# Kernel tuning notes

Hardware: AMD Instinct MI355X
Metric: run time of the kernel (lower is better)

The kernel has to match this reference:

```python
import jax, jax.numpy as jnp
import numpy as np

THRESH = 1.0   # snntorch Leaky default threshold
SLOPE = 25.0   # surrogate.fast_sigmoid(slope=25)
DIM_HEAD = 64
SCALE = DIM_HEAD ** -0.5

# snn.Leaky single step from zero membrane: mem = beta*0 + input = input,
# spike = heaviside(mem - threshold); backward uses fast_sigmoid surrogate.
@jax.custom_vjp
def spike_fn(mem):
    return (mem > THRESH).astype(mem.dtype)

def _spike_fwd(mem):
    return (mem > THRESH).astype(mem.dtype), mem

def _spike_bwd(mem, g):
    return (g / (SLOPE * jnp.abs(mem - THRESH) + 1.0) ** 2,)

spike_fn.defvjp(_spike_fwd, _spike_bwd)

def layer_norm2(x, gamma, beta, eps=1e-5):
    # torch F.layer_norm over x.shape[1:] (last two dims jointly);
    # gamma.repeat(rows,1) == broadcast of gamma over the row axis.
    m = x.mean(axis=(-2, -1), keepdims=True)
    v = x.var(axis=(-2, -1), keepdims=True)
    return (x - m) / jnp.sqrt(v + eps) * gamma + beta

def interp_linear(x, out_len):
    # F.interpolate(mode='linear', align_corners=False) over last axis
    L = x.shape[-1]
    j = jnp.arange(out_len, dtype=x.dtype)
    src = jnp.maximum((j + 0.5) * (L / out_len) - 0.5, 0.0)
    i0 = jnp.clip(jnp.floor(src).astype(jnp.int32), 0, L - 1)
    i1 = jnp.clip(i0 + 1, 0, L - 1)
    w = src - i0.astype(x.dtype)
    return x[..., i0] * (1.0 - w) + x[..., i1] * w

def setup_inputs() -> dict:
    key = jax.random.key(0)
    ks = jax.random.split(key, 8)
    H, N, DIM, HEADS, DH = 4, 512, 8192, 2, 64
    inner = HEADS * DH  # 128; H*inner = 512 (matches fc/conv dims)
    return {
        "pic": jax.random.normal(ks[0], (H, N, DIM), jnp.float32),
        "context": jax.random.normal(ks[1], (H, N, DIM), jnp.float32),
        "gamma": jnp.ones((DIM,), jnp.float32),
        "ln_beta": jnp.zeros((DIM,), jnp.float32),
        "W_pic": jax.random.normal(ks[2], (inner, DIM), jnp.float32) * 0.01,
        "b_pic": jnp.zeros((inner,), jnp.float32),
        "W_ctx": jax.random.normal(ks[3], (2 * DH, DIM), jnp.float32) * 0.01,
        "b_ctx": jnp.zeros((2 * DH,), jnp.float32),
        "conv1_w": jax.random.normal(ks[4], (32, N, 1), jnp.float32) * 0.04,
        "conv1_b": jnp.zeros((32,), jnp.float32),
        "conv2_w": jax.random.normal(ks[5], (1, 32, 1), jnp.float32) * 0.17,
        "conv2_b": jnp.zeros((1,), jnp.float32),
        "fc_w": jax.random.normal(ks[6], (N, N), jnp.float32) * 0.04,
        "fc_b": jnp.zeros((N,), jnp.float32),
    }

def reference(pic, context, gamma, ln_beta, W_pic, b_pic, W_ctx, b_ctx,
              conv1_w, conv1_b, conv2_w, conv2_b, fc_w, fc_b):
    pic = layer_norm2(pic, gamma, ln_beta)          # (H,N,DIM)
    context = layer_norm2(context, gamma, ln_beta)
    # num_steps = batch_size = 1: one SNN step, stack adds leading 'b'=1 axis
    ip_spk = spike_fn(pic)[None]                    # (1,H,N,DIM)
    ic_spk = spike_fn(context)[None]
    ip = (jnp.einsum('bhnd,od->bhno', ip_spk, W_pic) + b_pic) * SCALE  # (1,H,N,128)
    ctx = jnp.einsum('bhnd,od->bhno', ic_spk, W_ctx) + b_ctx           # (1,H,N,128)
    ic, V = jnp.split(ctx, 2, axis=-1)              # (1,H,N,64) each
    # einsum 'b h i d, b h i j -> b h i d': reduce j then broadcast-multiply
    sim = ip * ic.sum(-1, keepdims=True)            # (1,H,N,128)
    attn = jax.nn.softmax(sim, axis=-1)             # (sim - amax then softmax)
    # einsum 'b h i j, b h i d -> b h i j'
    out = attn * V.sum(-1, keepdims=True)           # (1,H,N,128)
    b, h, n, d = out.shape
    out = jnp.transpose(out, (0, 2, 1, 3)).reshape(b, n, h * d)  # (1,512,512)
    ip_sum = ip.sum(axis=3)                         # (1,H,512)
    # resnet: two kernel-size-1 Conv1d == channel-mixing matmuls
    o1 = jnp.einsum('bcl,oc->bol', out, conv1_w[:, :, 0]) + conv1_b[None, :, None]
    o1 = jnp.einsum('bcl,oc->bol', o1, conv2_w[:, :, 0]) + conv2_b[None, :, None]  # (1,1,512)
    o1 = o1 @ fc_w.T + fc_b                         # (1,1,512)
    o1 = o1 + ip_sum                                # broadcast -> (1,H,512)
    o1 = jnp.transpose(o1, (0, 2, 1))               # (1,512,H)
    o1 = interp_linear(o1, 64)                      # (1,512,64)
    ic_sum = ic.sum(axis=1)                         # (1,512,64)
    return jax.nn.relu(jax.nn.relu(o1) + ic_sum)
```

## Files before the change

kernel.cpp:

```cpp
#include <hip/hip_runtime.h>

typedef unsigned short ushort;
typedef unsigned int uint;
typedef __attribute__((ext_vector_type(8))) short short8v;
typedef __attribute__((ext_vector_type(4))) float floatx4;

#define DIMK   8192
#define NPER   512
#define NROWS  2048
#define NCOLS  128
#define KSPLIT 8
#define KCHUNK 1024
#define BK     64
#define BM     64
#define NIT    16
#define SLICE_ELEMS 4194304.0

static const size_t STATS_OFF = 0;
static const size_t O2_OFF    = 128;
static const size_t WB_OFF    = 4096;
static const size_t WB_BYTES  = (size_t)2 * 128 * DIMK * 2;
static const size_t P_OFF     = WB_OFF + WB_BYTES;
static const size_t P_BYTES   = (size_t)2 * KSPLIT * NROWS * NCOLS * 4;
static const size_t OUT2_OFF  = P_OFF + P_BYTES;
static const size_t IPSUM_OFF = OUT2_OFF + (size_t)512 * 512 * 4;
static const size_t CTXB_OFF  = IPSUM_OFF + (size_t)4 * 512 * 4;
static const size_t WS_NEED   = CTXB_OFF + (size_t)2048 * 64 * 4;

__device__ __forceinline__ ushort f2bf(float x) {
  uint u = __float_as_uint(x);
  return (ushort)((u + 0x7FFFu + ((u >> 16) & 1u)) >> 16);
}

__global__ __launch_bounds__(256) void k_wconv(const float* __restrict__ Wp,
                                               const float* __restrict__ Wc,
                                               ushort* __restrict__ Wb) {
  const size_t i = ((size_t)blockIdx.x * 256 + threadIdx.x) * 8;
  const size_t HALF = (size_t)128 * DIMK;
  const float* src = (i < HALF) ? (Wp + i) : (Wc + (i - HALF));
  float4 a = *(const float4*)src;
  float4 b = *(const float4*)(src + 4);
  short8v v;
  v[0] = (short)f2bf(a.x); v[1] = (short)f2bf(a.y);
  v[2] = (short)f2bf(a.z); v[3] = (short)f2bf(a.w);
  v[4] = (short)f2bf(b.x); v[5] = (short)f2bf(b.y);
  v[6] = (short)f2bf(b.z); v[7] = (short)f2bf(b.w);
  *(short8v*)&Wb[i] = v;
}

__global__ __launch_bounds__(256) void k_stats(const float* __restrict__ pic,
                                               const float* __restrict__ ctx,
                                               double* __restrict__ stats) {
  const int bid = blockIdx.x;
  const int tid = threadIdx.x;
  const int s = bid >> 8;
  const int c = bid & 255;
  const int t = s >> 2, h = s & 3;
  const float4* p4 = reinterpret_cast<const float4*>(
      (t ? ctx : pic) + (size_t)h * NPER * DIMK + (size_t)c * 16384) + tid;

  float4 va[4], vb[4];
  float sA[4] = {0.f, 0.f, 0.f, 0.f};
  float qA[4] = {0.f, 0.f, 0.f, 0.f};

  auto ACC = [&](const float4* v) {
#pragma unroll
    for (int j = 0; j < 4; ++j) {
      const float4 w = v[j];
      sA[j] += (w.x + w.y) + (w.z + w.w);
      qA[j] += (w.x * w.x + w.y * w.y) + (w.z * w.z + w.w * w.w);
    }
  };

#pragma unroll
  for (int j = 0; j < 4; ++j) va[j] = p4[256 * j];
#pragma unroll
  for (int j = 0; j < 4; ++j) vb[j] = p4[256 * (4 + j)];
  __builtin_amdgcn_sched_barrier(0);
  ACC(va);
#pragma unroll
  for (int j = 0; j < 4; ++j) va[j] = p4[256 * (8 + j)];
  __builtin_amdgcn_sched_barrier(0);
  ACC(vb);
#pragma unroll
  for (int j = 0; j < 4; ++j) vb[j] = p4[256 * (12 + j)];
  __builtin_amdgcn_sched_barrier(0);
  ACC(va);
  ACC(vb);

  float sum = (sA[0] + sA[1]) + (sA[2] + sA[3]);
  float sq  = (qA[0] + qA[1]) + (qA[2] + qA[3]);
#pragma unroll
  for (int d = 1; d < 64; d <<= 1) {
    sum += __shfl_xor(sum, d);
    sq  += __shfl_xor(sq, d);
  }
  __shared__ float ps[4], pq[4];
  const int w = tid >> 6;
  if ((tid & 63) == 0) { ps[w] = sum; pq[w] = sq; }
  __syncthreads();
  if (tid == 0) {
    double S = (double)ps[0] + (double)ps[1] + (double)ps[2] + (double)ps[3];
    double Q = (double)pq[0] + (double)pq[1] + (double)pq[2] + (double)pq[3];
    atomicAdd(&stats[2 * s], S);
    atomicAdd(&stats[2 * s + 1], Q);
  }
}

__global__ __launch_bounds__(256, 2) void k_gemm(const float* __restrict__ pic,
                                                 const float* __restrict__ ctxin,
                                                 const float* __restrict__ gamma,
                                                 const float* __restrict__ lnbeta,
                                                 const ushort* __restrict__ Wb,
                                                 const double* __restrict__ stats,
                                                 float* __restrict__ P) {
  const int tid  = threadIdx.x;
  const int lane = tid & 63;
  const int wv   = tid >> 6;
  const int wm   = wv >> 1, wn = wv & 1;
  const int bx = blockIdx.x, ky = blockIdx.y, t = blockIdx.z;
  const float*  A  = t ? ctxin : pic;
  const ushort* Wt = Wb + (size_t)t * 128 * DIMK;
  const int row0 = bx * BM;

  const int sidx = t * 4 + (bx >> 3);
  double su = stats[2 * sidx], qu = stats[2 * sidx + 1];
  double dmean = su * (1.0 / SLICE_ELEMS);
  const float mean = (float)dmean;
  const float var  = (float)(qu * (1.0 / SLICE_ELEMS) - dmean * dmean);
  const float rstd = rsqrtf(var + 1e-5f);

  __shared__ __align__(16) ushort Asl[2][BM * BK];
  __shared__ __align__(16) ushort Wsl[2][128 * BK];

  const int k8 = (tid & 7) * 8;
  const int r0 = tid >> 3;

  const int kg8 = (lane >> 4) << 3;
  int abase[2], axor[2], bbase[4], bxor[4];
#pragma unroll
  for (int m = 0; m < 2; ++m) {
    const int ra = wm * 32 + m * 16 + (lane & 15);
    abase[m] = ra * BK; axor[m] = (ra & 7) << 3;
  }
#pragma unroll
  for (int n = 0; n < 4; ++n) {
    const int rb = wn * 64 + n * 16 + (lane & 15);
    bbase[n] = rb * BK; bxor[n] = (rb & 7) << 3;
  }

  floatx4 acc[2][4];
  floatx4 zz = {0.f, 0.f, 0.f, 0.f};
#pragma unroll
  for (int m = 0; m < 2; ++m)
#pragma unroll
    for (int n = 0; n < 4; ++n) acc[m][n] = zz;

  float4 xa[2][2]; uint4 xw[4];
  float4 g0, g1, bb0, bb1;

  auto LOAD = [&](int it) {
    const int kb = ky * KCHUNK + it * BK;
    const float* gp = gamma  + kb + k8;
    const float* bp = lnbeta + kb + k8;
    g0 = *(const float4*)gp;  g1 = *(const float4*)(gp + 4);
    bb0 = *(const float4*)bp; bb1 = *(const float4*)(bp + 4);
#pragma unroll
    for (int c = 0; c < 2; ++c) {
      const float* ap = A + (size_t)(row0 + r0 + c * 32) * DIMK + kb + k8;
      xa[c][0] = *(const float4*)ap;
      xa[c][1] = *(const float4*)(ap + 4);
    }
#pragma unroll
    for (int c = 0; c < 4; ++c)
      xw[c] = *(const uint4*)(Wt + (size_t)(r0 + c * 32) * DIMK + kb + k8);
  };

  auto WRITE = [&](int buf) {
#pragma unroll
    for (int c = 0; c < 2; ++c) {
      const int r = r0 + c * 32;
      float xs[8] = {xa[c][0].x, xa[c][0].y, xa[c][0].z, xa[c][0].w,
                     xa[c][1].x, xa[c][1].y, xa[c][1].z, xa[c][1].w};
      float gs[8] = {g0.x, g0.y, g0.z, g0.w, g1.x, g1.y, g1.z, g1.w};
      float bs[8] = {bb0.x, bb0.y, bb0.z, bb0.w, bb1.x, bb1.y, bb1.z, bb1.w};
      short8v sv;
#pragma unroll
      for (int j = 0; j < 8; ++j)
        sv[j] = (short)(((xs[j] - mean) * rstd * gs[j] + bs[j] > 1.0f) ? 0x3F80 : 0);
      *(short8v*)&Asl[buf][r * BK + (k8 ^ ((r & 7) << 3))] = sv;
    }
#pragma unroll
    for (int c = 0; c < 4; ++c) {
      const int r = r0 + c * 32;
      *(uint4*)&Wsl[buf][r * BK + (k8 ^ ((r & 7) << 3))] = xw[c];
    }
  };

  auto COMPUTE = [&](int buf) {
#pragma unroll
    for (int ks = 0; ks < 2; ++ks) {
      short8v af[2], bfr[4];
#pragma unroll
      for (int m = 0; m < 2; ++m)
        af[m] = *(const short8v*)&Asl[buf][abase[m] + ((ks * 32 + kg8) ^ axor[m])];
#pragma unroll
      for (int n = 0; n < 4; ++n)
        bfr[n] = *(const short8v*)&Wsl[buf][bbase[n] + ((ks * 32 + kg8) ^ bxor[n])];
#pragma unroll
      for (int m = 0; m < 2; ++m)
#pragma unroll
        for (int n = 0; n < 4; ++n)
          acc[m][n] = __builtin_amdgcn_mfma_f32_16x16x32_bf16(af[m], bfr[n], acc[m][n], 0, 0, 0);
    }
  };

  LOAD(0);
  WRITE(0);
  __syncthreads();
#pragma unroll 2
  for (int it = 0; it < NIT - 1; ++it) {
    LOAD(it + 1);
    COMPUTE(it & 1);
    __syncthreads();
    WRITE((it + 1) & 1);
    __syncthreads();
  }
  COMPUTE((NIT - 1) & 1);

  float* Pt = P + ((size_t)(t * KSPLIT + ky) * NROWS + row0) * NCOLS;
#pragma unroll
  for (int m = 0; m < 2; ++m) {
    const int gr = wm * 32 + m * 16 + ((lane >> 4) << 2);
#pragma unroll
    for (int n = 0; n < 4; ++n) {
      const int gc = wn * 64 + n * 16 + (lane & 15);
#pragma unroll
      for (int j = 0; j < 4; ++j)
        Pt[(size_t)(gr + j) * NCOLS + gc] = acc[m][n][j];
    }
  }
}

__global__ __launch_bounds__(256) void k_row(const float* __restrict__ P,
                                             const float* __restrict__ b_pic,
                                             const float* __restrict__ b_ctx,
                                             float* __restrict__ out2,
                                             float* __restrict__ ipsum,
                                             float* __restrict__ ctxbuf) {
  const int tid = threadIdx.x;
  const int q = tid >> 5;
  const int u = tid & 31;
  const int r = blockIdx.x * 8 + q;
  const int o4 = u * 4;

  float4 ip = ((const float4*)b_pic)[u];
  float4 cv = ((const float4*)b_ctx)[u];
#pragma unroll
  for (int ks = 0; ks < KSPLIT; ++ks) {
    const float4 a = *(const float4*)&P[((size_t)ks * NROWS + r) * NCOLS + o4];
    const float4 b = *(const float4*)&P[((size_t)(KSPLIT + ks) * NROWS + r) * NCOLS + o4];
    ip.x += a.x; ip.y += a.y; ip.z += a.z; ip.w += a.w;
    cv.x += b.x; cv.y += b.y; cv.z += b.z; cv.w += b.w;
  }
  ip.x *= 0.125f; ip.y *= 0.125f; ip.z *= 0.125f; ip.w *= 0.125f;

  float clo = (u < 16) ? (cv.x + cv.y) + (cv.z + cv.w) : 0.f;
  float chi = (u >= 16) ? (cv.x + cv.y) + (cv.z + cv.w) : 0.f;
  float ipp = (ip.x + ip.y) + (ip.z + ip.w);
#pragma unroll
  for (int d = 1; d < 32; d <<= 1) {
    clo += __shfl_xor(clo, d);
    chi += __shfl_xor(chi, d);
    ipp += __shfl_xor(ipp, d);
  }
  const float ic_s = clo, v_s = chi;
  if (u == 0) ipsum[r] = ipp;

  float4 sim;
  sim.x = ip.x * ic_s; sim.y = ip.y * ic_s; sim.z = ip.z * ic_s; sim.w = ip.w * ic_s;
  float m = fmaxf(fmaxf(sim.x, sim.y), fmaxf(sim.z, sim.w));
#pragma unroll
  for (int d = 1; d < 32; d <<= 1) m = fmaxf(m, __shfl_xor(m, d));
  float4 e;
  e.x = __expf(sim.x - m); e.y = __expf(sim.y - m);
  e.z = __expf(sim.z - m); e.w = __expf(sim.w - m);
  float es = (e.x + e.y) + (e.z + e.w);
#pragma unroll
  for (int d = 1; d < 32; d <<= 1) es += __shfl_xor(es, d);
  const float sc = v_s / es;
  float4 outv;
  outv.x = e.x * sc; outv.y = e.y * sc; outv.z = e.z * sc; outv.w = e.w * sc;

  const int hh = r >> 9, n = r & 511;
  *(float4*)&out2[(size_t)n * 512 + hh * 128 + o4] = outv;
  if (u < 16) *(float4*)&ctxbuf[(size_t)r * 64 + o4] = cv;
}

__global__ __launch_bounds__(512) void k_mid(const float* __restrict__ out2,
                                             const float* __restrict__ c1w,
                                             const float* __restrict__ c1b,
                                             const float* __restrict__ c2w,
                                             const float* __restrict__ c2b,
                                             float* __restrict__ o2buf) {
  const int b = blockIdx.x;
  const int tid = threadIdx.x;
  __shared__ float wsh[64];
  __shared__ float c2s[32];
  if (tid < 32) c2s[tid] = c2w[tid];
  __syncthreads();
  if (tid < 64) {
    const int n = b * 64 + tid;
    float a = 0.f;
#pragma unroll
    for (int o = 0; o < 32; ++o) a += c2s[o] * c1w[o * 512 + n];
    wsh[tid] = a;
  }
  __syncthreads();
  float acc = 0.f;
#pragma unroll 8
  for (int ucnt = 0; ucnt < 64; ++ucnt)
    acc += out2[(size_t)(b * 64 + ucnt) * 512 + tid] * wsh[ucnt];
  if (b == 0) {
    float beff = c2b[0];
#pragma unroll
    for (int o = 0; o < 32; ++o) beff += c2s[o] * c1b[o];
    acc += beff;
  }
  atomicAdd(&o2buf[tid], acc);
}

__global__ __launch_bounds__(64) void k_final(const float* __restrict__ o2buf,
                                              const float* __restrict__ fcw,
                                              const float* __restrict__ fcb,
                                              const float* __restrict__ ipsum,
                                              const float* __restrict__ ctxbuf,
                                              float* __restrict__ out) {
  const int i = blockIdx.x;
  const int j = threadIdx.x;
  float a = 0.f;
#pragma unroll
  for (int uu = 0; uu < 8; ++uu) {
    const int k = j * 8 + uu;
    a += o2buf[k] * fcw[(size_t)i * 512 + k];
  }
#pragma unroll
  for (int d = 1; d < 64; d <<= 1) a += __shfl_xor(a, d);
  const float o3 = a + fcb[i];

  float src = (j + 0.5f) * (4.0f / 64.0f) - 0.5f;
  src = fmaxf(src, 0.0f);
  int i0 = (int)floorf(src);
  if (i0 > 3) i0 = 3;
  const int i1 = (i0 + 1 < 3) ? i0 + 1 : 3;
  const float w = src - (float)i0;

  const float v0 = o3 + ipsum[i0 * 512 + i];
  const float v1 = o3 + ipsum[i1 * 512 + i];
  float v = v0 * (1.0f - w) + v1 * w;
  v = fmaxf(v, 0.0f);

  float ics = 0.f;
#pragma unroll
  for (int hh2 = 0; hh2 < 4; ++hh2) ics += ctxbuf[((size_t)hh2 * 512 + i) * 64 + j];
  out[(size_t)i * 64 + j] = fmaxf(v + ics, 0.0f);
}

extern "C" void kernel_launch(void* const* d_in, const int* in_sizes, int n_in,
                              void* d_out, int out_size, void* d_ws, size_t ws_size,
                              hipStream_t stream) {
  const float* pic    = (const float*)d_in[0];
  const float* ctx    = (const float*)d_in[1];
  const float* gamma  = (const float*)d_in[2];
  const float* lnbeta = (const float*)d_in[3];
  const float* Wp     = (const float*)d_in[4];
  const float* bp     = (const float*)d_in[5];
  const float* Wc     = (const float*)d_in[6];
  const float* bc     = (const float*)d_in[7];
  const float* c1w    = (const float*)d_in[8];
  const float* c1b    = (const float*)d_in[9];
  const float* c2w    = (const float*)d_in[10];
  const float* c2b    = (const float*)d_in[11];
  const float* fcw    = (const float*)d_in[12];
  const float* fcb    = (const float*)d_in[13];
  float* out = (float*)d_out;

  if (ws_size < WS_NEED) return;

  char* ws = (char*)d_ws;
  double* stats = (double*)(ws + STATS_OFF);
  float* o2buf  = (float*)(ws + O2_OFF);
  ushort* Wb    = (ushort*)(ws + WB_OFF);
  float* P      = (float*)(ws + P_OFF);
  float* out2   = (float*)(ws + OUT2_OFF);
  float* ipsum  = (float*)(ws + IPSUM_OFF);
  float* ctxbuf = (float*)(ws + CTXB_OFF);

  hipMemsetAsync(ws, 0, 128 + 512 * 4, stream);
  k_wconv<<<1024, 256, 0, stream>>>(Wp, Wc, Wb);
  k_stats<<<2048, 256, 0, stream>>>(pic, ctx, stats);
  k_gemm<<<dim3(32, KSPLIT, 2), 256, 0, stream>>>(pic, ctx, gamma, lnbeta, Wb, stats, P);
  k_row<<<256, 256, 0, stream>>>(P, bp, bc, out2, ipsum, ctxbuf);
  k_mid<<<8, 512, 0, stream>>>(out2, c1w, c1b, c2w, c2b, o2buf);
  k_final<<<512, 64, 0, stream>>>(o2buf, fcw, fcb, ipsum, ctxbuf, out);
}
```

Before: 247.9 us.

## Halve GEMM row tile, raise occupancy, fold weight conversion into stats kernel

The GEMM row tile is halved from 64 to 32, so the grid doubles and each wave keeps a quarter as many accumulators. Launch bounds are raised so more blocks fit per CU, which is meant to hide global-load latency on the fp32 activation stream. One of the two barriers in the double-buffered loop is dropped, since the write targets the buffer not being read. The separate weight-to-bf16 conversion kernel becomes extra blocks of the stats kernel, saving a launch. In exchange, each block reuses the bf16 weight tile over fewer rows, so weight traffic through the caches doubles.

```diff
diff --git a/kernel.cpp b/kernel.cpp
--- a/kernel.cpp
+++ b/kernel.cpp
@@ -12,7 +12,7 @@
 #define KSPLIT 8
 #define KCHUNK 1024
 #define BK     64
-#define BM     64
+#define BM     32
 #define NIT    16
 #define SLICE_ELEMS 4194304.0
 
@@ -32,27 +32,28 @@
   return (ushort)((u + 0x7FFFu + ((u >> 16) & 1u)) >> 16);
 }
 
-__global__ __launch_bounds__(256) void k_wconv(const float* __restrict__ Wp,
-                                               const float* __restrict__ Wc,
-                                               ushort* __restrict__ Wb) {
-  const size_t i = ((size_t)blockIdx.x * 256 + threadIdx.x) * 8;
-  const size_t HALF = (size_t)128 * DIMK;
-  const float* src = (i < HALF) ? (Wp + i) : (Wc + (i - HALF));
-  float4 a = *(const float4*)src;
-  float4 b = *(const float4*)(src + 4);
-  short8v v;
-  v[0] = (short)f2bf(a.x); v[1] = (short)f2bf(a.y);
-  v[2] = (short)f2bf(a.z); v[3] = (short)f2bf(a.w);
-  v[4] = (short)f2bf(b.x); v[5] = (short)f2bf(b.y);
-  v[6] = (short)f2bf(b.z); v[7] = (short)f2bf(b.w);
-  *(short8v*)&Wb[i] = v;
-}
-
 __global__ __launch_bounds__(256) void k_stats(const float* __restrict__ pic,
                                                const float* __restrict__ ctx,
-                                               double* __restrict__ stats) {
+                                               const float* __restrict__ Wp,
+                                               const float* __restrict__ Wc,
+                                               double* __restrict__ stats,
+                                               ushort* __restrict__ Wb) {
   const int bid = blockIdx.x;
   const int tid = threadIdx.x;
+  if (bid >= 2048) {
+    const size_t i = ((size_t)(bid - 2048) * 256 + tid) * 8;
+    const size_t HALF = (size_t)128 * DIMK;
+    const float* src = (i < HALF) ? (Wp + i) : (Wc + (i - HALF));
+    float4 a = *(const float4*)src;
+    float4 b = *(const float4*)(src + 4);
+    short8v v;
+    v[0] = (short)f2bf(a.x); v[1] = (short)f2bf(a.y);
+    v[2] = (short)f2bf(a.z); v[3] = (short)f2bf(a.w);
+    v[4] = (short)f2bf(b.x); v[5] = (short)f2bf(b.y);
+    v[6] = (short)f2bf(b.z); v[7] = (short)f2bf(b.w);
+    *(short8v*)&Wb[i] = v;
+    return;
+  }
   const int s = bid >> 8;
   const int c = bid & 255;
   const int t = s >> 2, h = s & 3;
@@ -107,7 +108,7 @@
   }
 }
 
-__global__ __launch_bounds__(256, 2) void k_gemm(const float* __restrict__ pic,
+__global__ __launch_bounds__(256, 4) void k_gemm(const float* __restrict__ pic,
                                                  const float* __restrict__ ctxin,
                                                  const float* __restrict__ gamma,
                                                  const float* __restrict__ lnbeta,
@@ -123,7 +124,7 @@
   const ushort* Wt = Wb + (size_t)t * 128 * DIMK;
   const int row0 = bx * BM;
 
-  const int sidx = t * 4 + (bx >> 3);
+  const int sidx = t * 4 + (bx >> 4);
   double su = stats[2 * sidx], qu = stats[2 * sidx + 1];
   double dmean = su * (1.0 / SLICE_ELEMS);
   const float mean = (float)dmean;
@@ -137,11 +138,10 @@
   const int r0 = tid >> 3;
 
   const int kg8 = (lane >> 4) << 3;
-  int abase[2], axor[2], bbase[4], bxor[4];
-#pragma unroll
-  for (int m = 0; m < 2; ++m) {
-    const int ra = wm * 32 + m * 16 + (lane & 15);
-    abase[m] = ra * BK; axor[m] = (ra & 7) << 3;
+  int abase, axor, bbase[4], bxor[4];
+  {
+    const int ra = wm * 16 + (lane & 15);
+    abase = ra * BK; axor = (ra & 7) << 3;
   }
 #pragma unroll
   for (int n = 0; n < 4; ++n) {
@@ -149,14 +149,12 @@
     bbase[n] = rb * BK; bxor[n] = (rb & 7) << 3;
   }
 
-  floatx4 acc[2][4];
+  floatx4 acc[4];
   floatx4 zz = {0.f, 0.f, 0.f, 0.f};
 #pragma unroll
-  for (int m = 0; m < 2; ++m)
-#pragma unroll
-    for (int n = 0; n < 4; ++n) acc[m][n] = zz;
-
-  float4 xa[2][2]; uint4 xw[4];
+  for (int n = 0; n < 4; ++n) acc[n] = zz;
+
+  float4 xa[2]; uint4 xw[4];
   float4 g0, g1, bb0, bb1;
 
   auto LOAD = [&](int it) {
@@ -165,23 +163,19 @@
     const float* bp = lnbeta + kb + k8;
     g0 = *(const float4*)gp;  g1 = *(const float4*)(gp + 4);
     bb0 = *(const float4*)bp; bb1 = *(const float4*)(bp + 4);
-#pragma unroll
-    for (int c = 0; c < 2; ++c) {
-      const float* ap = A + (size_t)(row0 + r0 + c * 32) * DIMK + kb + k8;
-      xa[c][0] = *(const float4*)ap;
-      xa[c][1] = *(const float4*)(ap + 4);
-    }
+    const float* ap = A + (size_t)(row0 + r0) * DIMK + kb + k8;
+    xa[0] = *(const float4*)ap;
+    xa[1] = *(const float4*)(ap + 4);
 #pragma unroll
     for (int c = 0; c < 4; ++c)
       xw[c] = *(const uint4*)(Wt + (size_t)(r0 + c * 32) * DIMK + kb + k8);
   };
 
   auto WRITE = [&](int buf) {
-#pragma unroll
-    for (int c = 0; c < 2; ++c) {
-      const int r = r0 + c * 32;
-      float xs[8] = {xa[c][0].x, xa[c][0].y, xa[c][0].z, xa[c][0].w,
-                     xa[c][1].x, xa[c][1].y, xa[c][1].z, xa[c][1].w};
+    {
+      const int r = r0;
+      float xs[8] = {xa[0].x, xa[0].y, xa[0].z, xa[0].w,
+                     xa[1].x, xa[1].y, xa[1].z, xa[1].w};
       float gs[8] = {g0.x, g0.y, g0.z, g0.w, g1.x, g1.y, g1.z, g1.w};
       float bs[8] = {bb0.x, bb0.y, bb0.z, bb0.w, bb1.x, bb1.y, bb1.z, bb1.w};
       short8v sv;
@@ -200,18 +194,14 @@
   auto COMPUTE = [&](int buf) {
 #pragma unroll
     for (int ks = 0; ks < 2; ++ks) {
-      short8v af[2], bfr[4];
-#pragma unroll
-      for (int m = 0; m < 2; ++m)
-        af[m] = *(const short8v*)&Asl[buf][abase[m] + ((ks * 32 + kg8) ^ axor[m])];
+      short8v af, bfr[4];
+      af = *(const short8v*)&Asl[buf][abase + ((ks * 32 + kg8) ^ axor)];
 #pragma unroll
       for (int n = 0; n < 4; ++n)
         bfr[n] = *(const short8v*)&Wsl[buf][bbase[n] + ((ks * 32 + kg8) ^ bxor[n])];
 #pragma unroll
-      for (int m = 0; m < 2; ++m)
-#pragma unroll
-        for (int n = 0; n < 4; ++n)
-          acc[m][n] = __builtin_amdgcn_mfma_f32_16x16x32_bf16(af[m], bfr[n], acc[m][n], 0, 0, 0);
+      for (int n = 0; n < 4; ++n)
+        acc[n] = __builtin_amdgcn_mfma_f32_16x16x32_bf16(af, bfr[n], acc[n], 0, 0, 0);
     }
   };
 
@@ -222,23 +212,19 @@
   for (int it = 0; it < NIT - 1; ++it) {
     LOAD(it + 1);
     COMPUTE(it & 1);
-    __syncthreads();
     WRITE((it + 1) & 1);
     __syncthreads();
   }
   COMPUTE((NIT - 1) & 1);
 
   float* Pt = P + ((size_t)(t * KSPLIT + ky) * NROWS + row0) * NCOLS;
-#pragma unroll
-  for (int m = 0; m < 2; ++m) {
-    const int gr = wm * 32 + m * 16 + ((lane >> 4) << 2);
-#pragma unroll
-    for (int n = 0; n < 4; ++n) {
-      const int gc = wn * 64 + n * 16 + (lane & 15);
-#pragma unroll
-      for (int j = 0; j < 4; ++j)
-        Pt[(size_t)(gr + j) * NCOLS + gc] = acc[m][n][j];
-    }
+  const int gr = wm * 16 + ((lane >> 4) << 2);
+#pragma unroll
+  for (int n = 0; n < 4; ++n) {
+    const int gc = wn * 64 + n * 16 + (lane & 15);
+#pragma unroll
+    for (int j = 0; j < 4; ++j)
+      Pt[(size_t)(gr + j) * NCOLS + gc] = acc[n][j];
   }
 }
 
@@ -397,9 +383,8 @@
   float* ctxbuf = (float*)(ws + CTXB_OFF);
 
   hipMemsetAsync(ws, 0, 128 + 512 * 4, stream);
-  k_wconv<<<1024, 256, 0, stream>>>(Wp, Wc, Wb);
-  k_stats<<<2048, 256, 0, stream>>>(pic, ctx, stats);
-  k_gemm<<<dim3(32, KSPLIT, 2), 256, 0, stream>>>(pic, ctx, gamma, lnbeta, Wb, stats, P);
+  k_stats<<<3072, 256, 0, stream>>>(pic, ctx, Wp, Wc, stats, Wb);
+  k_gemm<<<dim3(64, KSPLIT, 2), 256, 0, stream>>>(pic, ctx, gamma, lnbeta, Wb, stats, P);
   k_row<<<256, 256, 0, stream>>>(P, bp, bc, out2, ipsum, ctxbuf);
   k_mid<<<8, 512, 0, stream>>>(out2, c1w, c1b, c2w, c2b, o2buf);
   k_final<<<512, 64, 0, stream>>>(o2buf, fcw, fcb, ipsum, ctxbuf, out);
```

Result: slower. 270.8 us (+9.2%).

## Fold weight conversion into stats kernel, drop GEMM barrier, coalesce partial stores

Applied to the files above, without the earlier changes.

The fp32-to-bf16 weight conversion now runs as extra blocks of the stats kernel, which removes one launch and lets both jobs overlap. The stats kernel issues all 16 float4 loads up front instead of staging them through two buffers. The split-K GEMM drops a redundant barrier in its double-buffered main loop. Its epilogue now stages the accumulators through a padded LDS tile so partial results go to global memory as coalesced float4 rows. The extra ~33KB of LDS and the larger register footprint in the stats kernel may reduce occupancy.

```diff
diff --git a/kernel.cpp b/kernel.cpp
--- a/kernel.cpp
+++ b/kernel.cpp
@@ -32,61 +32,50 @@
   return (ushort)((u + 0x7FFFu + ((u >> 16) & 1u)) >> 16);
 }
 
-__global__ __launch_bounds__(256) void k_wconv(const float* __restrict__ Wp,
-                                               const float* __restrict__ Wc,
-                                               ushort* __restrict__ Wb) {
-  const size_t i = ((size_t)blockIdx.x * 256 + threadIdx.x) * 8;
-  const size_t HALF = (size_t)128 * DIMK;
-  const float* src = (i < HALF) ? (Wp + i) : (Wc + (i - HALF));
-  float4 a = *(const float4*)src;
-  float4 b = *(const float4*)(src + 4);
-  short8v v;
-  v[0] = (short)f2bf(a.x); v[1] = (short)f2bf(a.y);
-  v[2] = (short)f2bf(a.z); v[3] = (short)f2bf(a.w);
-  v[4] = (short)f2bf(b.x); v[5] = (short)f2bf(b.y);
-  v[6] = (short)f2bf(b.z); v[7] = (short)f2bf(b.w);
-  *(short8v*)&Wb[i] = v;
-}
-
 __global__ __launch_bounds__(256) void k_stats(const float* __restrict__ pic,
                                                const float* __restrict__ ctx,
-                                               double* __restrict__ stats) {
+                                               const float* __restrict__ Wp,
+                                               const float* __restrict__ Wc,
+                                               double* __restrict__ stats,
+                                               ushort* __restrict__ Wb) {
   const int bid = blockIdx.x;
   const int tid = threadIdx.x;
+  if (bid >= 2048) {
+    const size_t i = ((size_t)(bid - 2048) * 256 + tid) * 8;
+    const size_t HALF = (size_t)128 * DIMK;
+    const float* src = (i < HALF) ? (Wp + i) : (Wc + (i - HALF));
+    float4 a = *(const float4*)src;
+    float4 b = *(const float4*)(src + 4);
+    short8v v;
+    v[0] = (short)f2bf(a.x); v[1] = (short)f2bf(a.y);
+    v[2] = (short)f2bf(a.z); v[3] = (short)f2bf(a.w);
+    v[4] = (short)f2bf(b.x); v[5] = (short)f2bf(b.y);
+    v[6] = (short)f2bf(b.z); v[7] = (short)f2bf(b.w);
+    *(short8v*)&Wb[i] = v;
+    return;
+  }
   const int s = bid >> 8;
   const int c = bid & 255;
   const int t = s >> 2, h = s & 3;
   const float4* p4 = reinterpret_cast<const float4*>(
       (t ? ctx : pic) + (size_t)h * NPER * DIMK + (size_t)c * 16384) + tid;
 
-  float4 va[4], vb[4];
+  float4 v[16];
+#pragma unroll
+  for (int j = 0; j < 16; ++j) v[j] = p4[256 * j];
+  __builtin_amdgcn_sched_barrier(0);
+
   float sA[4] = {0.f, 0.f, 0.f, 0.f};
   float qA[4] = {0.f, 0.f, 0.f, 0.f};
-
-  auto ACC = [&](const float4* v) {
-#pragma unroll
-    for (int j = 0; j < 4; ++j) {
-      const float4 w = v[j];
-      sA[j] += (w.x + w.y) + (w.z + w.w);
-      qA[j] += (w.x * w.x + w.y * w.y) + (w.z * w.z + w.w * w.w);
-    }
-  };
-
-#pragma unroll
-  for (int j = 0; j < 4; ++j) va[j] = p4[256 * j];
-#pragma unroll
-  for (int j = 0; j < 4; ++j) vb[j] = p4[256 * (4 + j)];
-  __builtin_amdgcn_sched_barrier(0);
-  ACC(va);
-#pragma unroll
-  for (int j = 0; j < 4; ++j) va[j] = p4[256 * (8 + j)];
-  __builtin_amdgcn_sched_barrier(0);
-  ACC(vb);
-#pragma unroll
-  for (int j = 0; j < 4; ++j) vb[j] = p4[256 * (12 + j)];
-  __builtin_amdgcn_sched_barrier(0);
-  ACC(va);
-  ACC(vb);
+#pragma unroll
+  for (int j = 0; j < 16; j += 4) {
+#pragma unroll
+    for (int u = 0; u < 4; ++u) {
+      const float4 w = v[j + u];
+      sA[u] += (w.x + w.y) + (w.z + w.w);
+      qA[u] += (w.x * w.x + w.y * w.y) + (w.z * w.z + w.w * w.w);
+    }
+  }
 
   float sum = (sA[0] + sA[1]) + (sA[2] + sA[3]);
   float sq  = (qA[0] + qA[1]) + (qA[2] + qA[3]);
@@ -132,6 +121,7 @@
 
   __shared__ __align__(16) ushort Asl[2][BM * BK];
   __shared__ __align__(16) ushort Wsl[2][128 * BK];
+  __shared__ __align__(16) float  Cst[BM][132];
 
   const int k8 = (tid & 7) * 8;
   const int r0 = tid >> 3;
@@ -222,13 +212,11 @@
   for (int it = 0; it < NIT - 1; ++it) {
     LOAD(it + 1);
     COMPUTE(it & 1);
-    __syncthreads();
     WRITE((it + 1) & 1);
     __syncthreads();
   }
   COMPUTE((NIT - 1) & 1);
 
-  float* Pt = P + ((size_t)(t * KSPLIT + ky) * NROWS + row0) * NCOLS;
 #pragma unroll
   for (int m = 0; m < 2; ++m) {
     const int gr = wm * 32 + m * 16 + ((lane >> 4) << 2);
@@ -237,9 +225,17 @@
       const int gc = wn * 64 + n * 16 + (lane & 15);
 #pragma unroll
       for (int j = 0; j < 4; ++j)
-        Pt[(size_t)(gr + j) * NCOLS + gc] = acc[m][n][j];
-    }
-  }
+        Cst[gr + j][gc] = acc[m][n][j];
+    }
+  }
+  __syncthreads();
+  float* Pt = P + ((size_t)(t * KSPLIT + ky) * NROWS + row0) * NCOLS;
+  const int rr = tid >> 2;
+  const int cq = (tid & 3) * 32;
+  float* dst = Pt + (size_t)rr * NCOLS + cq;
+#pragma unroll
+  for (int i = 0; i < 8; ++i)
+    *(float4*)(dst + i * 4) = *(const float4*)&Cst[rr][cq + i * 4];
 }
 
 __global__ __launch_bounds__(256) void k_row(const float* __restrict__ P,
@@ -397,8 +393,7 @@
   float* ctxbuf = (float*)(ws + CTXB_OFF);
 
   hipMemsetAsync(ws, 0, 128 + 512 * 4, stream);
-  k_wconv<<<1024, 256, 0, stream>>>(Wp, Wc, Wb);
-  k_stats<<<2048, 256, 0, stream>>>(pic, ctx, stats);
+  k_stats<<<3072, 256, 0, stream>>>(pic, ctx, Wp, Wc, stats, Wb);
   k_gemm<<<dim3(32, KSPLIT, 2), 256, 0, stream>>>(pic, ctx, gamma, lnbeta, Wb, stats, P);
   k_row<<<256, 256, 0, stream>>>(P, bp, bc, out2, ipsum, ctxbuf);
   k_mid<<<8, 512, 0, stream>>>(out2, c1w, c1b, c2w, c2b, o2buf);
```

Measured after the change: 265.1 us. 1.07x slower.
